# Performance work log

Hardware: AMD Instinct MI355X
Metric: run time of the kernel (lower is better)

## Reference

```python
import jax, jax.numpy as jnp
import numpy as np

N_EMBD = 1024
N_HEAD = 16
HEAD_DIM = N_EMBD // N_HEAD


def setup_inputs() -> dict:
    key = jax.random.key(0)
    k1, k2, k3 = jax.random.split(key, 3)
    x = jax.random.normal(k1, (2, 2048, N_EMBD), dtype=jnp.float32)
    # torch nn.Linear(in, out) weight has shape (out, in); y = x @ W.T
    w_qkv = jax.random.normal(k2, (3 * N_EMBD, N_EMBD), dtype=jnp.float32) * (1.0 / np.sqrt(N_EMBD))
    w_proj = jax.random.normal(k3, (N_EMBD, N_EMBD), dtype=jnp.float32) * (1.0 / np.sqrt(N_EMBD))
    return {"x": x, "w_qkv": w_qkv, "w_proj": w_proj}


def reference(x, w_qkv, w_proj):
    B, T, C = x.shape
    qkv = jnp.einsum('btc,dc->btd', x, w_qkv)  # [B,T,3C]
    q, k, v = jnp.split(qkv, 3, axis=2)
    # [B,H,T,hd]
    q = q.reshape(B, T, N_HEAD, HEAD_DIM).transpose(0, 2, 1, 3)
    k = k.reshape(B, T, N_HEAD, HEAD_DIM).transpose(0, 2, 1, 3)
    v = v.reshape(B, T, N_HEAD, HEAD_DIM).transpose(0, 2, 1, 3)
    att = jnp.einsum('bhqd,bhkd->bhqk', q, k) / jnp.sqrt(jnp.float32(HEAD_DIM))
    causal = jnp.tril(jnp.ones((T, T), dtype=bool))  # [T,T]
    att = jnp.where(causal[None, None], att, -jnp.inf)
    att = jax.nn.softmax(att, axis=-1)
    y = jnp.einsum('bhqk,bhkd->bhqd', att, v)
    y = y.transpose(0, 2, 1, 3).reshape(B, T, C)
    return jnp.einsum('btc,dc->btd', y, w_proj)
```

## Files before the change

kernel.cpp:

```cpp
#include <hip/hip_runtime.h>
#include <stdint.h>


typedef unsigned short u16;
typedef __bf16 bf16_t;
typedef bf16_t bf16x8 __attribute__((ext_vector_type(8)));
typedef float f32x4 __attribute__((ext_vector_type(4)));
typedef float f32x16 __attribute__((ext_vector_type(16)));

__device__ __forceinline__ u16 f2bf(float f) {
  return __builtin_bit_cast(u16, (bf16_t)f);
}

__device__ __forceinline__ float hexp2(float x) {
  float r;
  asm("v_exp_f32 %0, %1" : "=v"(r) : "v"(x));
  return r;
}
__device__ __forceinline__ uint32_t cvtpk(float lo, float hi) {
  uint32_t d;
  asm("v_cvt_pk_bf16_f32 %0, %1, %2" : "=v"(d) : "v"(lo), "v"(hi));
  return d;
}
__device__ __forceinline__ void plswap(uint32_t& a, uint32_t& b) {
  asm("v_permlane32_swap_b32 %0, %1" : "+v"(a), "+v"(b));
}

template<int CC>
__device__ __forceinline__ bf16x8 mkPfrag(const float* p) {
  uint32_t A1 = cvtpk(p[8 * CC + 0], p[8 * CC + 1]);
  uint32_t A2 = cvtpk(p[8 * CC + 2], p[8 * CC + 3]);
  uint32_t B1 = cvtpk(p[8 * CC + 4], p[8 * CC + 5]);
  uint32_t B2 = cvtpk(p[8 * CC + 6], p[8 * CC + 7]);
  plswap(A1, B1);
  plswap(A2, B2);
  union { uint32_t u[4]; bf16x8 v; } r;
  r.u[0] = A1; r.u[1] = A2; r.u[2] = B1; r.u[3] = B2;
  return r.v;
}

__device__ __forceinline__ void gload_lds16(const void* g, void* l) {
  __builtin_amdgcn_global_load_lds(
      (const __attribute__((address_space(1))) uint32_t*)(uint64_t)g,
      (__attribute__((address_space(3))) uint32_t*)(uint32_t)(uint64_t)l,
      16, 0, 0);
}

__global__ void cast_all(const float* __restrict__ x, const float* __restrict__ wq,
                         const float* __restrict__ wp, u16* __restrict__ xb,
                         u16* __restrict__ wqb, u16* __restrict__ wpb) {
  int i = blockIdx.x * blockDim.x + threadIdx.x;
  const float* s; u16* d; int off;
  if (i < 1048576)            { s = x;  d = xb;  off = i; }
  else if (i < 1048576 + 786432) { s = wq; d = wqb; off = i - 1048576; }
  else                        { s = wp; d = wpb; off = i - (1048576 + 786432); }
  float4 f = reinterpret_cast<const float4*>(s)[off];
  ushort4 o;
  o.x = f2bf(f.x); o.y = f2bf(f.y); o.z = f2bf(f.z); o.w = f2bf(f.w);
  reinterpret_cast<ushort4*>(d)[off] = o;
}

template<int MODE, int BM>
__global__ void gemm_bt(const u16* __restrict__ A, const u16* __restrict__ Bm,
                        u16* __restrict__ qb, u16* __restrict__ kb, u16* __restrict__ vb,
                        float* __restrict__ outf) {
  constexpr int NF = (BM == 128) ? 4 : 2;
  __shared__ __attribute__((aligned(16))) u16 SMEM[BM * 64 + 128 * 64];
  const int tid = threadIdx.x;
  const int lane = tid & 63;
  const int w = tid >> 6;
  const int wr = (BM == 128) ? (w >> 1) : 0;
  const int wc = (BM == 128) ? (w & 1) : w;
  const int g = lane >> 4, r = lane & 15;
  const int tn = blockIdx.x, tm = blockIdx.y;

  f32x4 acc[4][NF] = {};

  const char* Ab = (const char*)(A + (size_t)tm * BM * 1024);
  const char* Bb = (const char*)(Bm + (size_t)tn * 128 * 1024);
  char* AsB = (char*)SMEM;
  char* BsB = AsB + BM * 128;

  for (int k0 = 0; k0 < 1024; k0 += 64) {
#pragma unroll
    for (int i = 0; i < BM / 32; ++i) {
      const int L = (i * 256 + tid) * 16;
      const int row = L >> 7;
      const int colb = (L & 127) ^ ((row & 7) << 4);
      gload_lds16(Ab + (size_t)row * 2048 + k0 * 2 + colb, AsB + L);
    }
#pragma unroll
    for (int i = 0; i < 4; ++i) {
      const int L = (i * 256 + tid) * 16;
      const int row = L >> 7;
      const int colb = (L & 127) ^ ((row & 7) << 4);
      gload_lds16(Bb + (size_t)row * 2048 + k0 * 2 + colb, BsB + L);
    }
    __syncthreads();
#pragma unroll
    for (int kk = 0; kk < 2; ++kk) {
      bf16x8 a[4], b[NF];
#pragma unroll
      for (int m = 0; m < 4; ++m) {
        const int rowA = wr * 64 + m * 16 + r;
        const int kbyt = (kk * 64 + g * 16) ^ ((rowA & 7) << 4);
        a[m] = *(const bf16x8*)(AsB + rowA * 128 + kbyt);
      }
#pragma unroll
      for (int n = 0; n < NF; ++n) {
        const int rowB = wc * (NF * 16) + n * 16 + r;
        const int kbyt = (kk * 64 + g * 16) ^ ((rowB & 7) << 4);
        b[n] = *(const bf16x8*)(BsB + rowB * 128 + kbyt);
      }
      __builtin_amdgcn_s_setprio(1);
#pragma unroll
      for (int m = 0; m < 4; ++m)
#pragma unroll
        for (int n = 0; n < NF; ++n)
          acc[m][n] = __builtin_amdgcn_mfma_f32_16x16x32_bf16(a[m], b[n], acc[m][n], 0, 0, 0);
      __builtin_amdgcn_s_setprio(0);
    }
    __syncthreads();
  }

  const int mrow0 = tm * BM + wr * 64;
  const int ncol0 = tn * 128 + wc * (NF * 16);

  if (MODE == 1) {
#pragma unroll
    for (int m = 0; m < 4; ++m)
#pragma unroll
      for (int n = 0; n < NF; ++n) {
        const int nc = ncol0 + n * 16 + r;
#pragma unroll
        for (int j = 0; j < 4; ++j) {
          const int mr = mrow0 + m * 16 + g * 4 + j;
          outf[(size_t)mr * 1024 + nc] = acc[m][n][j];
        }
      }
  } else if (MODE == 0) {
    const int sel = (blockIdx.x * 128) >> 10;
    const float qscl = (sel == 0) ? 0.18033688f : 1.0f;
    if (sel < 2) {
      u16* dst = (sel == 0) ? qb : kb;
#pragma unroll
      for (int m = 0; m < 4; ++m)
#pragma unroll
        for (int n = 0; n < NF; ++n) {
          const int nc = (ncol0 + n * 16 + r) & 1023;
          const int h = nc >> 6, d = nc & 63;
#pragma unroll
          for (int j = 0; j < 4; ++j) {
            const int mr = mrow0 + m * 16 + g * 4 + j;
            const int bb = mr >> 11, t = mr & 2047;
            dst[((size_t)(bb * 16 + h) * 2048 + t) * 64 + d] = f2bf(acc[m][n][j] * qscl);
          }
        }
    } else {
      u16* Wv = SMEM + w * 4096;
#pragma unroll
      for (int m = 0; m < 4; ++m)
#pragma unroll
        for (int n = 0; n < NF; ++n) {
          const int dl = n * 16 + r;
          uint32_t lo = cvtpk(acc[m][n][0], acc[m][n][1]);
          uint32_t hi2 = cvtpk(acc[m][n][2], acc[m][n][3]);
          char* p = (char*)Wv + dl * 128 + ((m * 32 + g * 8) ^ ((dl & 7) << 4));
          *(uint32_t*)p = lo;
          *(uint32_t*)(p + 4) = hi2;
        }
      asm volatile("s_waitcnt lgkmcnt(0)" ::: "memory");
      __builtin_amdgcn_sched_barrier(0);
      const int hh = (ncol0 - 2048) >> 6;
      const int t0 = mrow0 & 2047;
      const int bb2 = mrow0 >> 11;
      u16* vdst = vb + ((size_t)(bb2 * 16 + hh) * 64) * 2048 + t0;
#pragma unroll
      for (int rd = 0; rd < 8; ++rd) {
        const int dl = rd * 8 + (lane >> 3);
        const int tb = lane & 7;
        const char* src = (char*)Wv + dl * 128 + ((tb ^ (dl & 7)) << 4);
        *(uint4*)(vdst + (size_t)dl * 2048 + tb * 8) = *(const uint4*)src;
      }
    }
  }
}

__global__ __launch_bounds__(256, 2)
void attn_fwd(const u16* __restrict__ qb, const u16* __restrict__ kb,
              const u16* __restrict__ vb, u16* __restrict__ yb) {
  __shared__ __attribute__((aligned(16))) u16 Ks[2][128 * 64];
  __shared__ __attribute__((aligned(16))) u16 Vs[2][64 * 128];
  __shared__ __attribute__((aligned(16))) float Linv[4][32];
  const int tid = threadIdx.x;
  const int lane = tid & 63;
  const int w = tid >> 6;
  const int hi = lane >> 5;
  const int q5 = lane & 31;
  const int hi4 = hi * 4;
  const int bh = blockIdx.x;
  const int bb = bh >> 4, h = bh & 15;
  const int base = (blockIdx.y + bh) & 15;
  const int a = (base < 8) ? 2 * base : 31 - 2 * base;
  const int qb0 = a * 128;
  const int qw = qb0 + w * 32;
  const int qg = qw + q5;

  const char* Kb = (const char*)(kb + (size_t)bh * (2048 * 64));
  const char* Vb = (const char*)(vb + (size_t)bh * (64 * 2048));
  const u16* Q = qb + (size_t)bh * (2048 * 64);

  bf16x8 qf[4];
#pragma unroll
  for (int f = 0; f < 4; ++f)
    qf[f] = *(const bf16x8*)(&Q[(size_t)qg * 64 + f * 16 + hi * 8]);

  f32x16 o0 = {}, o1 = {};
  float psum = 0.0f;

  const int nph = a + 1;
  const int swzK = (q5 & 7) << 4;
  const int swzV = (q5 & 15) << 4;

  auto stage = [&](int p, int buf) {
#pragma unroll
    for (int i = 0; i < 4; ++i) {
      const int L = (i * 256 + tid) * 16;
      const int row = L >> 7;
      const int colb = (L & 127) ^ ((row & 7) << 4);
      gload_lds16(Kb + ((size_t)p * 128 + row) * 128 + colb, (char*)Ks[buf] + L);
    }
#pragma unroll
    for (int i = 0; i < 4; ++i) {
      const int L = (i * 256 + tid) * 16;
      const int row = L >> 8;
      const int colb = (L & 255) ^ ((row & 15) << 4);
      gload_lds16(Vb + (size_t)row * 4096 + (size_t)p * 256 + colb, (char*)Vs[buf] + L);
    }
  };

  auto compute = [&](int p, const char* KsB, const char* VsB) {
#pragma unroll
    for (int hh = 0; hh < 4; ++hh) {
      const int kh = p * 128 + hh * 32;
      if (kh <= qw + 31) {
        f32x16 s = {};
        __builtin_amdgcn_s_setprio(1);
#pragma unroll
        for (int f = 0; f < 4; ++f) {
          bf16x8 ka = *(const bf16x8*)(KsB + (hh * 32 + q5) * 128 + ((f * 32 + hi * 16) ^ swzK));
          s = __builtin_amdgcn_mfma_f32_32x32x16_bf16(ka, qf[f], s, 0, 0, 0);
        }
        __builtin_amdgcn_s_setprio(0);

        float pv[16];
        if (kh + 31 > qw) {
#pragma unroll
          for (int i = 0; i < 16; ++i) {
            const int kl = (i & 3) + 8 * (i >> 2) + hi4;
            float e = hexp2(s[i]);
            pv[i] = (kh + kl <= qg) ? e : 0.0f;
            psum += pv[i];
          }
        } else {
#pragma unroll
          for (int i = 0; i < 16; ++i) {
            pv[i] = hexp2(s[i]);
            psum += pv[i];
          }
        }

        bf16x8 pf0 = mkPfrag<0>(pv);
        bf16x8 pf1 = mkPfrag<1>(pv);

        __builtin_amdgcn_s_setprio(1);
#pragma unroll
        for (int c = 0; c < 2; ++c) {
          const int cc = hh * 2 + c;
          const int cb = cc * 32 + hi * 16;
          bf16x8 v0f = *(const bf16x8*)(VsB + q5 * 256 + (cb ^ swzV));
          bf16x8 v1f = *(const bf16x8*)(VsB + (32 + q5) * 256 + (cb ^ swzV));
          const bf16x8 pf = c ? pf1 : pf0;
          o0 = __builtin_amdgcn_mfma_f32_32x32x16_bf16(pf, v0f, o0, 0, 0, 0);
          o1 = __builtin_amdgcn_mfma_f32_32x32x16_bf16(pf, v1f, o1, 0, 0, 0);
        }
        __builtin_amdgcn_s_setprio(0);
      }
    }
  };

  stage(0, 0);
  for (int t = 0; t < nph; ++t) {
    const int pn = (t + 1 < nph) ? t + 1 : 0;
    stage(pn, (t + 1) & 1);
    asm volatile("s_waitcnt vmcnt(8)" ::: "memory");
    __builtin_amdgcn_s_barrier();
    __builtin_amdgcn_sched_barrier(0);
    compute(t, (const char*)Ks[t & 1], (const char*)Vs[t & 1]);
    __builtin_amdgcn_sched_barrier(0);
    __builtin_amdgcn_s_barrier();
  }

  const float tot = psum + __shfl_xor(psum, 32);
  if (lane < 32) Linv[w][q5] = 1.0f / tot;
  asm volatile("s_waitcnt lgkmcnt(0)" ::: "memory");
  __builtin_amdgcn_sched_barrier(0);
  f32x4 lv[4];
#pragma unroll
  for (int r2 = 0; r2 < 4; ++r2)
    lv[r2] = *(const f32x4*)(&Linv[w][r2 * 8 + hi4]);

#pragma unroll
  for (int reg = 0; reg < 16; ++reg) {
    const int r4 = reg & 3, r2 = reg >> 2;
    const float li = lv[r2][r4];
    const int trow = qw + r4 + 8 * r2 + hi4;
    const size_t bpos = ((size_t)(bb * 2048 + trow)) * 1024 + h * 64 + q5;
    yb[bpos]      = f2bf(o0[reg] * li);
    yb[bpos + 32] = f2bf(o1[reg] * li);
  }
}

extern "C" void kernel_launch(void* const* d_in, const int* in_sizes, int n_in,
                              void* d_out, int out_size, void* d_ws, size_t ws_size,
                              hipStream_t stream) {
  const float* x     = (const float*)d_in[0];
  const float* wqkv  = (const float*)d_in[1];
  const float* wproj = (const float*)d_in[2];
  float* out = (float*)d_out;
  char* ws = (char*)d_ws;
  u16* xb     = (u16*)(ws + (size_t)(0u  << 20));
  u16* wqkvb  = (u16*)(ws + (size_t)(8u  << 20));
  u16* wprojb = (u16*)(ws + (size_t)(14u << 20));
  u16* qb     = (u16*)(ws + (size_t)(16u << 20));
  u16* kb     = (u16*)(ws + (size_t)(24u << 20));
  u16* vb     = (u16*)(ws + (size_t)(32u << 20));
  u16* yb     = (u16*)(ws + (size_t)(40u << 20));

  cast_all<<<8192, 256, 0, stream>>>(x, wqkv, wproj, xb, wqkvb, wprojb);

  gemm_bt<0, 128><<<dim3(24, 32), 256, 0, stream>>>(xb, wqkvb, qb, kb, vb, nullptr);
  attn_fwd<<<dim3(32, 16), 256, 0, stream>>>(qb, kb, vb, yb);
  gemm_bt<1, 64><<<dim3(8, 64), 256, 0, stream>>>(yb, wprojb, nullptr, nullptr, nullptr, out);
}
```

Before: 93.40 us.

## Rewrite QKV GEMM with 256x256 tiles and double-buffered LDS pipeline

The QKV projection GEMM moves to a dedicated kernel with 512 threads, 256x256 output tiles, K-step 64 and double-buffered global-to-LDS loads, so the next tile's load overlaps MFMA work through vmcnt waits. Fragment loads and MFMA groups are interleaved in quadrants with barriers and priority hints. The output GEMM becomes its own simplified kernel. In exchange, the grid shrinks to 192 blocks, which may underfill the GPU's 256 CUs, and the larger tiles use 128KB of LDS per block.

Result: slower. 99.02 us (+6.0%).

```diff
diff --git a/kernel.cpp b/kernel.cpp
--- a/kernel.cpp
+++ b/kernel.cpp
@@ -60,30 +60,198 @@
   reinterpret_cast<ushort4*>(d)[off] = o;
 }
 
-template<int MODE, int BM>
-__global__ void gemm_bt(const u16* __restrict__ A, const u16* __restrict__ Bm,
-                        u16* __restrict__ qb, u16* __restrict__ kb, u16* __restrict__ vb,
-                        float* __restrict__ outf) {
-  constexpr int NF = (BM == 128) ? 4 : 2;
-  __shared__ __attribute__((aligned(16))) u16 SMEM[BM * 64 + 128 * 64];
+__global__ __launch_bounds__(512, 1)
+void gemm_qkv(const u16* __restrict__ A, const u16* __restrict__ Bm,
+              u16* __restrict__ qb, u16* __restrict__ kb, u16* __restrict__ vb) {
+  __shared__ __attribute__((aligned(16))) u16 SMEM[65536];
   const int tid = threadIdx.x;
   const int lane = tid & 63;
   const int w = tid >> 6;
-  const int wr = (BM == 128) ? (w >> 1) : 0;
-  const int wc = (BM == 128) ? (w & 1) : w;
+  const int wm = w >> 2, wn = w & 3;
   const int g = lane >> 4, r = lane & 15;
   const int tn = blockIdx.x, tm = blockIdx.y;
 
+  const char* Ab = (const char*)A + (size_t)tm * 256 * 2048;
+  const char* Bb = (const char*)Bm + (size_t)tn * 256 * 2048;
+
+  f32x4 acc[8][4] = {};
+
+  auto stage = [&](int T, int buf) {
+    const int k0b = T * 128;
+    char* AsD = (char*)(SMEM + buf * 16384);
+    char* BsD = (char*)(SMEM + 32768 + buf * 16384);
+#pragma unroll
+    for (int i = 0; i < 4; ++i) {
+      const int L = (i * 512 + tid) * 16;
+      const int row = L >> 7;
+      const int colb = (L & 127) ^ ((row & 7) << 4);
+      gload_lds16(Ab + (size_t)row * 2048 + k0b + colb, AsD + L);
+      gload_lds16(Bb + (size_t)row * 2048 + k0b + colb, BsD + L);
+    }
+  };
+
+  stage(0, 0);
+  for (int T = 0; T < 16; ++T) {
+    const int cur = T & 1;
+    if (T + 1 < 16) {
+      stage(T + 1, cur ^ 1);
+      asm volatile("s_waitcnt vmcnt(8)" ::: "memory");
+    } else {
+      asm volatile("s_waitcnt vmcnt(0)" ::: "memory");
+    }
+    __builtin_amdgcn_s_barrier();
+    __builtin_amdgcn_sched_barrier(0);
+
+    const char* Ac = (const char*)(SMEM + cur * 16384);
+    const char* Bc = (const char*)(SMEM + 32768 + cur * 16384);
+
+    bf16x8 a0[4][2], a1[4][2], b0[2][2], b1[2][2];
+
+#pragma unroll
+    for (int m = 0; m < 4; ++m) {
+      const int rowA = wm * 128 + m * 16 + r;
+#pragma unroll
+      for (int kk = 0; kk < 2; ++kk)
+        a0[m][kk] = *(const bf16x8*)(Ac + rowA * 128 + ((kk * 64 + g * 16) ^ ((rowA & 7) << 4)));
+    }
+#pragma unroll
+    for (int n = 0; n < 2; ++n) {
+      const int rowB = wn * 64 + n * 16 + r;
+#pragma unroll
+      for (int kk = 0; kk < 2; ++kk)
+        b0[n][kk] = *(const bf16x8*)(Bc + rowB * 128 + ((kk * 64 + g * 16) ^ ((rowB & 7) << 4)));
+    }
+    __builtin_amdgcn_s_barrier();
+    __builtin_amdgcn_s_setprio(1);
+#pragma unroll
+    for (int m = 0; m < 4; ++m)
+#pragma unroll
+      for (int n = 0; n < 2; ++n)
+#pragma unroll
+        for (int kk = 0; kk < 2; ++kk)
+          acc[m][n] = __builtin_amdgcn_mfma_f32_16x16x32_bf16(a0[m][kk], b0[n][kk], acc[m][n], 0, 0, 0);
+    __builtin_amdgcn_s_setprio(0);
+    __builtin_amdgcn_s_barrier();
+
+#pragma unroll
+    for (int n = 0; n < 2; ++n) {
+      const int rowB = wn * 64 + (n + 2) * 16 + r;
+#pragma unroll
+      for (int kk = 0; kk < 2; ++kk)
+        b1[n][kk] = *(const bf16x8*)(Bc + rowB * 128 + ((kk * 64 + g * 16) ^ ((rowB & 7) << 4)));
+    }
+    __builtin_amdgcn_s_barrier();
+    __builtin_amdgcn_s_setprio(1);
+#pragma unroll
+    for (int m = 0; m < 4; ++m)
+#pragma unroll
+      for (int n = 0; n < 2; ++n)
+#pragma unroll
+        for (int kk = 0; kk < 2; ++kk)
+          acc[m][n + 2] = __builtin_amdgcn_mfma_f32_16x16x32_bf16(a0[m][kk], b1[n][kk], acc[m][n + 2], 0, 0, 0);
+    __builtin_amdgcn_s_setprio(0);
+    __builtin_amdgcn_s_barrier();
+
+#pragma unroll
+    for (int m = 0; m < 4; ++m) {
+      const int rowA = wm * 128 + (m + 4) * 16 + r;
+#pragma unroll
+      for (int kk = 0; kk < 2; ++kk)
+        a1[m][kk] = *(const bf16x8*)(Ac + rowA * 128 + ((kk * 64 + g * 16) ^ ((rowA & 7) << 4)));
+    }
+    __builtin_amdgcn_s_barrier();
+    __builtin_amdgcn_s_setprio(1);
+#pragma unroll
+    for (int m = 0; m < 4; ++m)
+#pragma unroll
+      for (int n = 0; n < 2; ++n)
+#pragma unroll
+        for (int kk = 0; kk < 2; ++kk)
+          acc[m + 4][n + 2] = __builtin_amdgcn_mfma_f32_16x16x32_bf16(a1[m][kk], b1[n][kk], acc[m + 4][n + 2], 0, 0, 0);
+    __builtin_amdgcn_s_setprio(0);
+    __builtin_amdgcn_s_barrier();
+
+    __builtin_amdgcn_s_setprio(1);
+#pragma unroll
+    for (int m = 0; m < 4; ++m)
+#pragma unroll
+      for (int n = 0; n < 2; ++n)
+#pragma unroll
+        for (int kk = 0; kk < 2; ++kk)
+          acc[m + 4][n] = __builtin_amdgcn_mfma_f32_16x16x32_bf16(a1[m][kk], b0[n][kk], acc[m + 4][n], 0, 0, 0);
+    __builtin_amdgcn_s_setprio(0);
+    __builtin_amdgcn_s_barrier();
+    __builtin_amdgcn_sched_barrier(0);
+  }
+
+  const int mrow0 = tm * 256 + wm * 128;
+  const int ncol0 = tn * 256 + wn * 64;
+  const int sel = tn >> 2;
+
+  if (sel < 2) {
+    u16* dst = (sel == 0) ? qb : kb;
+    const float qscl = (sel == 0) ? 0.18033688f : 1.0f;
+#pragma unroll
+    for (int m = 0; m < 8; ++m)
+#pragma unroll
+      for (int n = 0; n < 4; ++n) {
+        const int nc = (ncol0 + n * 16 + r) & 1023;
+        const int h = nc >> 6, d = nc & 63;
+#pragma unroll
+        for (int j = 0; j < 4; ++j) {
+          const int mr = mrow0 + m * 16 + g * 4 + j;
+          const int bb = mr >> 11, t = mr & 2047;
+          dst[((size_t)(bb * 16 + h) * 2048 + t) * 64 + d] = f2bf(acc[m][n][j] * qscl);
+        }
+      }
+  } else {
+    u16* Wv = SMEM + w * 8192;
+#pragma unroll
+    for (int m = 0; m < 8; ++m)
+#pragma unroll
+      for (int n = 0; n < 4; ++n) {
+        const int dl = n * 16 + r;
+        uint32_t lo = cvtpk(acc[m][n][0], acc[m][n][1]);
+        uint32_t hi2 = cvtpk(acc[m][n][2], acc[m][n][3]);
+        char* p = (char*)Wv + dl * 256 + ((m * 32 + g * 8) ^ ((dl & 15) << 4));
+        *(uint32_t*)p = lo;
+        *(uint32_t*)(p + 4) = hi2;
+      }
+    asm volatile("s_waitcnt lgkmcnt(0)" ::: "memory");
+    __builtin_amdgcn_sched_barrier(0);
+    const int h = (tn - 8) * 4 + wn;
+    const int bb = mrow0 >> 11, t0 = mrow0 & 2047;
+    u16* vdst = vb + ((size_t)(bb * 16 + h) * 64) * 2048 + t0;
+#pragma unroll
+    for (int rd = 0; rd < 16; ++rd) {
+      const int dl = rd * 4 + (lane >> 4);
+      const int tb = lane & 15;
+      const char* src = (char*)Wv + dl * 256 + ((tb * 16) ^ ((dl & 15) << 4));
+      *(uint4*)(vdst + (size_t)dl * 2048 + tb * 8) = *(const uint4*)src;
+    }
+  }
+}
+
+__global__ void gemm_out(const u16* __restrict__ A, const u16* __restrict__ Bm,
+                         float* __restrict__ outf) {
+  constexpr int NF = 2;
+  __shared__ __attribute__((aligned(16))) u16 SMEM[64 * 64 + 128 * 64];
+  const int tid = threadIdx.x;
+  const int lane = tid & 63;
+  const int w = tid >> 6;
+  const int g = lane >> 4, r = lane & 15;
+  const int tn = blockIdx.x, tm = blockIdx.y;
+
   f32x4 acc[4][NF] = {};
 
-  const char* Ab = (const char*)(A + (size_t)tm * BM * 1024);
+  const char* Ab = (const char*)(A + (size_t)tm * 64 * 1024);
   const char* Bb = (const char*)(Bm + (size_t)tn * 128 * 1024);
   char* AsB = (char*)SMEM;
-  char* BsB = AsB + BM * 128;
+  char* BsB = AsB + 64 * 128;
 
   for (int k0 = 0; k0 < 1024; k0 += 64) {
 #pragma unroll
-    for (int i = 0; i < BM / 32; ++i) {
+    for (int i = 0; i < 2; ++i) {
       const int L = (i * 256 + tid) * 16;
       const int row = L >> 7;
       const int colb = (L & 127) ^ ((row & 7) << 4);
@@ -102,13 +270,13 @@
       bf16x8 a[4], b[NF];
 #pragma unroll
       for (int m = 0; m < 4; ++m) {
-        const int rowA = wr * 64 + m * 16 + r;
+        const int rowA = m * 16 + r;
         const int kbyt = (kk * 64 + g * 16) ^ ((rowA & 7) << 4);
         a[m] = *(const bf16x8*)(AsB + rowA * 128 + kbyt);
       }
 #pragma unroll
       for (int n = 0; n < NF; ++n) {
-        const int rowB = wc * (NF * 16) + n * 16 + r;
+        const int rowB = w * (NF * 16) + n * 16 + r;
         const int kbyt = (kk * 64 + g * 16) ^ ((rowB & 7) << 4);
         b[n] = *(const bf16x8*)(BsB + rowB * 128 + kbyt);
       }
@@ -123,67 +291,19 @@
     __syncthreads();
   }
 
-  const int mrow0 = tm * BM + wr * 64;
-  const int ncol0 = tn * 128 + wc * (NF * 16);
-
-  if (MODE == 1) {
-#pragma unroll
-    for (int m = 0; m < 4; ++m)
-#pragma unroll
-      for (int n = 0; n < NF; ++n) {
-        const int nc = ncol0 + n * 16 + r;
-#pragma unroll
-        for (int j = 0; j < 4; ++j) {
-          const int mr = mrow0 + m * 16 + g * 4 + j;
-          outf[(size_t)mr * 1024 + nc] = acc[m][n][j];
-        }
-      }
-  } else if (MODE == 0) {
-    const int sel = (blockIdx.x * 128) >> 10;
-    const float qscl = (sel == 0) ? 0.18033688f : 1.0f;
-    if (sel < 2) {
-      u16* dst = (sel == 0) ? qb : kb;
-#pragma unroll
-      for (int m = 0; m < 4; ++m)
-#pragma unroll
-        for (int n = 0; n < NF; ++n) {
-          const int nc = (ncol0 + n * 16 + r) & 1023;
-          const int h = nc >> 6, d = nc & 63;
-#pragma unroll
-          for (int j = 0; j < 4; ++j) {
-            const int mr = mrow0 + m * 16 + g * 4 + j;
-            const int bb = mr >> 11, t = mr & 2047;
-            dst[((size_t)(bb * 16 + h) * 2048 + t) * 64 + d] = f2bf(acc[m][n][j] * qscl);
-          }
-        }
-    } else {
-      u16* Wv = SMEM + w * 4096;
-#pragma unroll
-      for (int m = 0; m < 4; ++m)
-#pragma unroll
-        for (int n = 0; n < NF; ++n) {
-          const int dl = n * 16 + r;
-          uint32_t lo = cvtpk(acc[m][n][0], acc[m][n][1]);
-          uint32_t hi2 = cvtpk(acc[m][n][2], acc[m][n][3]);
-          char* p = (char*)Wv + dl * 128 + ((m * 32 + g * 8) ^ ((dl & 7) << 4));
-          *(uint32_t*)p = lo;
-          *(uint32_t*)(p + 4) = hi2;
-        }
-      asm volatile("s_waitcnt lgkmcnt(0)" ::: "memory");
-      __builtin_amdgcn_sched_barrier(0);
-      const int hh = (ncol0 - 2048) >> 6;
-      const int t0 = mrow0 & 2047;
-      const int bb2 = mrow0 >> 11;
-      u16* vdst = vb + ((size_t)(bb2 * 16 + hh) * 64) * 2048 + t0;
-#pragma unroll
-      for (int rd = 0; rd < 8; ++rd) {
-        const int dl = rd * 8 + (lane >> 3);
-        const int tb = lane & 7;
-        const char* src = (char*)Wv + dl * 128 + ((tb ^ (dl & 7)) << 4);
-        *(uint4*)(vdst + (size_t)dl * 2048 + tb * 8) = *(const uint4*)src;
-      }
-    }
-  }
+  const int mrow0 = tm * 64;
+  const int ncol0 = tn * 128 + w * (NF * 16);
+#pragma unroll
+  for (int m = 0; m < 4; ++m)
+#pragma unroll
+    for (int n = 0; n < NF; ++n) {
+      const int nc = ncol0 + n * 16 + r;
+#pragma unroll
+      for (int j = 0; j < 4; ++j) {
+        const int mr = mrow0 + m * 16 + g * 4 + j;
+        outf[(size_t)mr * 1024 + nc] = acc[m][n][j];
+      }
+    }
 }
 
 __global__ __launch_bounds__(256, 2)
@@ -339,7 +459,7 @@
 
   cast_all<<<8192, 256, 0, stream>>>(x, wqkv, wproj, xb, wqkvb, wprojb);
 
-  gemm_bt<0, 128><<<dim3(24, 32), 256, 0, stream>>>(xb, wqkvb, qb, kb, vb, nullptr);
+  gemm_qkv<<<dim3(12, 16), 512, 0, stream>>>(xb, wqkvb, qb, kb, vb);
   attn_fwd<<<dim3(32, 16), 256, 0, stream>>>(qb, kb, vb, yb);
-  gemm_bt<1, 64><<<dim3(8, 64), 256, 0, stream>>>(yb, wprojb, nullptr, nullptr, nullptr, out);
-}
+  gemm_out<<<dim3(8, 64), 256, 0, stream>>>(yb, wprojb, out);
+}
```
